# Optimization experiments

Hardware: AMD Instinct MI355X
Metric: run time of the kernel (lower is better)

The kernel has to match this reference:

```python
import jax, jax.numpy as jnp
import numpy as np

BATCH, T, N_STATE, N_IN, N_OUT = 256, 4096, 32, 8, 8
DT = 1e-3


def setup_inputs() -> dict:
    key = jax.random.key(0)
    k_u, k_x0, k_A, k_B, k_C, k_D = jax.random.split(key, 6)
    t = jnp.arange(T, dtype=jnp.float32) * DT
    u = jax.random.normal(k_u, (BATCH, T, N_IN), dtype=jnp.float32)
    x0 = jax.random.normal(k_x0, (BATCH, N_STATE), dtype=jnp.float32)
    # Stable-ish LTI system parameters
    A = (0.1 / np.sqrt(N_STATE)) * jax.random.normal(k_A, (N_STATE, N_STATE), dtype=jnp.float32) - 0.5 * jnp.eye(N_STATE, dtype=jnp.float32)
    B = jax.random.normal(k_B, (N_STATE, N_IN), dtype=jnp.float32) / np.sqrt(N_IN)
    C = jax.random.normal(k_C, (N_OUT, N_STATE), dtype=jnp.float32) / np.sqrt(N_STATE)
    D = jax.random.normal(k_D, (N_OUT, N_IN), dtype=jnp.float32) / np.sqrt(N_IN)
    return {"t": t, "u": u, "x0": x0, "A": A, "B": B, "C": C, "D": D}


def _dopri5_solve(t, u, x0, A, B):
    """Fixed-step Dopri5 (Dormand-Prince 5th order) on a uniform grid.

    Mirrors diffrax.diffeqsolve(Dopri5, ConstantStepSize, dt0=t[1], saveat=ts=t):
    one RK step per grid interval. u is evaluated at stage times via linear
    interpolation between grid samples.
    """
    dt = t[1] - t[0]

    def f(x, uu):  # vector field: dx = A x + B u
        return x @ A.T + uu @ B.T

    ut = jnp.swapaxes(u, 0, 1)  # [T, BATCH, N_IN]

    def step(x, uu):
        u0, u1 = uu
        du = u1 - u0
        k1 = f(x, u0)
        k2 = f(x + dt * (0.2 * k1), u0 + 0.2 * du)
        k3 = f(x + dt * (3.0 / 40.0 * k1 + 9.0 / 40.0 * k2), u0 + 0.3 * du)
        k4 = f(x + dt * (44.0 / 45.0 * k1 - 56.0 / 15.0 * k2 + 32.0 / 9.0 * k3), u0 + 0.8 * du)
        k5 = f(x + dt * (19372.0 / 6561.0 * k1 - 25360.0 / 2187.0 * k2 + 64448.0 / 6561.0 * k3 - 212.0 / 729.0 * k4), u0 + (8.0 / 9.0) * du)
        k6 = f(x + dt * (9017.0 / 3168.0 * k1 - 355.0 / 33.0 * k2 + 46732.0 / 5247.0 * k3 + 49.0 / 176.0 * k4 - 5103.0 / 18656.0 * k5), u1)
        xn = x + dt * (35.0 / 384.0 * k1 + 500.0 / 1113.0 * k3 + 125.0 / 192.0 * k4 - 2187.0 / 6784.0 * k5 + 11.0 / 84.0 * k6)
        return xn, xn

    _, xs_rest = jax.lax.scan(step, x0, (ut[:-1], ut[1:]))
    xs = jnp.concatenate([x0[None], xs_rest], axis=0)  # [T, BATCH, N_STATE]
    return jnp.swapaxes(xs, 0, 1)  # [BATCH, T, N_STATE]


def reference(t, u, x0, A, B, C, D):
    xs = _dopri5_solve(t, u, x0, A, B)          # state trajectory [BATCH, T, N_STATE]
    ys = xs @ C.T + u @ D.T                      # output y = C x + D u, [BATCH, T, N_OUT]
    return xs, ys
```

## Files before the change

### kernel.cpp

```cpp
#include <hip/hip_runtime.h>

#define BATCH 256
#define TT 4096
#define NS 32
#define NI 8
#define NO 8
#define LCH 64
#define NCHUNKS 64

#define WS_M  0
#define WS_N0 1024
#define WS_N1 1280
#define WS_ML 1536
#define WS_V  2560
#define WS_S  (2560 + BATCH * NCHUNKS * NS)

__device__ __forceinline__ float dot4(float4 a, float4 b) {
    return a.x * b.x + a.y * b.y + a.z * b.z + a.w * b.w;
}
__device__ __forceinline__ float4 ld4(const float* p) { return *(const float4*)p; }

__global__ __launch_bounds__(256) void k_pre(const float* __restrict__ tarr,
                                             const float* __restrict__ A,
                                             const float* __restrict__ B,
                                             float* __restrict__ ws) {
    __shared__ float sA[NS * NS], sB[NS * NI];
    __shared__ float Ka[6][NS * NS];
    __shared__ float Kb[6][NS * NI];
    __shared__ float Kc[6][NS * NI];
    __shared__ float Sa[NS * NS], Sb[NS * NI], Sc[NS * NI];
    __shared__ float Pq[2][NS * NS];

    const int tid = threadIdx.x;
    const float dt = tarr[1] - tarr[0];

    for (int e = tid; e < NS * NS; e += 256) sA[e] = A[e];
    for (int e = tid; e < NS * NI; e += 256) sB[e] = B[e];
    __syncthreads();
    for (int e = tid; e < NS * NS; e += 256) Ka[0][e] = sA[e];
    for (int e = tid; e < NS * NI; e += 256) { Kb[0][e] = sB[e]; Kc[0][e] = 0.f; }
    __syncthreads();

    const float atab[5][5] = {
        {0.2f, 0.f, 0.f, 0.f, 0.f},
        {3.f / 40.f, 9.f / 40.f, 0.f, 0.f, 0.f},
        {44.f / 45.f, -56.f / 15.f, 32.f / 9.f, 0.f, 0.f},
        {19372.f / 6561.f, -25360.f / 2187.f, 64448.f / 6561.f, -212.f / 729.f, 0.f},
        {9017.f / 3168.f, -355.f / 33.f, 46732.f / 5247.f, 49.f / 176.f, -5103.f / 18656.f}};
    const float ctab[6] = {0.f, 0.2f, 0.3f, 0.8f, 8.f / 9.f, 1.f};

    for (int st = 1; st <= 5; ++st) {
        for (int e = tid; e < NS * NS; e += 256) {
            float acc = 0.f;
            for (int j = 0; j < st; ++j) acc += atab[st - 1][j] * Ka[j][e];
            Sa[e] = acc;
        }
        for (int e = tid; e < NS * NI; e += 256) {
            float ab = 0.f, ac = 0.f;
            for (int j = 0; j < st; ++j) {
                ab += atab[st - 1][j] * Kb[j][e];
                ac += atab[st - 1][j] * Kc[j][e];
            }
            Sb[e] = ab; Sc[e] = ac;
        }
        __syncthreads();
        {
            const int j = tid & 31, ig = tid >> 5;
            for (int r = 0; r < 4; ++r) {
                const int row = ig + 8 * r;
                float acc = 0.f;
                for (int k = 0; k < NS; ++k) acc += sA[row * NS + k] * Sa[k * NS + j];
                Ka[st][row * NS + j] = sA[row * NS + j] + dt * acc;
            }
            const int jb = tid & 7, rb = tid >> 3;
            float ab = 0.f, ac = 0.f;
            for (int k = 0; k < NS; ++k) {
                ab += sA[rb * NS + k] * Sb[k * NI + jb];
                ac += sA[rb * NS + k] * Sc[k * NI + jb];
            }
            Kb[st][rb * NI + jb] = sB[rb * NI + jb] + dt * ab;
            Kc[st][rb * NI + jb] = ctab[st] * sB[rb * NI + jb] + dt * ac;
        }
        __syncthreads();
    }

    const float btab[6] = {35.f / 384.f, 0.f, 500.f / 1113.f, 125.f / 192.f,
                           -2187.f / 6784.f, 11.f / 84.f};
    for (int e = tid; e < NS * NS; e += 256) {
        float acc = 0.f;
        for (int i2 = 0; i2 < 6; ++i2) acc += btab[i2] * Ka[i2][e];
        const float m = dt * acc + (((e / NS) == (e % NS)) ? 1.f : 0.f);
        ws[WS_M + e] = m;
        Pq[0][e] = m;
    }
    for (int e = tid; e < NS * NI; e += 256) {
        float ap = 0.f, aq = 0.f;
        for (int i2 = 0; i2 < 6; ++i2) {
            ap += btab[i2] * Kb[i2][e];
            aq += btab[i2] * Kc[i2][e];
        }
        const float P = dt * ap, Q = dt * aq;
        ws[WS_N0 + e] = P - Q;
        ws[WS_N1 + e] = Q;
    }
    __syncthreads();

    int cur = 0;
    for (int itq = 0; itq < 6; ++itq) {
        const int j = tid & 31, ig = tid >> 5;
        for (int r = 0; r < 4; ++r) {
            const int row = ig + 8 * r;
            float acc = 0.f;
            for (int k = 0; k < NS; ++k) acc += Pq[cur][row * NS + k] * Pq[cur][k * NS + j];
            Pq[cur ^ 1][row * NS + j] = acc;
        }
        __syncthreads();
        cur ^= 1;
    }
    for (int e = tid; e < NS * NS; e += 256) ws[WS_ML + e] = Pq[cur][e];
}

template <bool P3>
__global__ __launch_bounds__(64, 1) void k_phase13(const float* __restrict__ u,
                                                   float* __restrict__ ws,
                                                   float* __restrict__ out,
                                                   const float* __restrict__ Cc,
                                                   const float* __restrict__ Dd) {
    const float* M = ws + WS_M;
    const float* N0 = ws + WS_N0;
    const float* N1 = ws + WS_N1;

    const int nch = P3 ? NCHUNKS : (NCHUNKS - 1);
    const int task = blockIdx.x;
    const int c = task % nch, g = task / nch;
    const int l = threadIdx.x;
    const int beta = l >> 3, s8 = l & 7;
    const int b = g * 8 + beta;

    float4 mq[4][8];
#pragma unroll
    for (int r = 0; r < 4; ++r)
#pragma unroll
        for (int jj = 0; jj < 8; ++jj) mq[r][jj] = ld4(M + (4 * s8 + r) * NS + 4 * jj);

    float4 n0q[4][2], n1q[4][2];
#pragma unroll
    for (int r = 0; r < 4; ++r) {
        n0q[r][0] = ld4(N0 + (4 * s8 + r) * NI);
        n0q[r][1] = ld4(N0 + (4 * s8 + r) * NI + 4);
        n1q[r][0] = ld4(N1 + (4 * s8 + r) * NI);
        n1q[r][1] = ld4(N1 + (4 * s8 + r) * NI + 4);
    }

    float4 cq[8], dq[2];
    if constexpr (P3) {
#pragma unroll
        for (int jj = 0; jj < 8; ++jj) cq[jj] = ld4(Cc + s8 * NS + 4 * jj);
        dq[0] = ld4(Dd + s8 * NI);
        dq[1] = ld4(Dd + s8 * NI + 4);
    }

    __shared__ float4 xb[2][8 * 9];

    const int t0 = c * LCH;
    const float* ub = u + (size_t)b * TT * NI;
    float4 u0a = ld4(ub + t0 * NI), u0b = ld4(ub + t0 * NI + 4);

    float4 mine;
    if constexpr (P3)
        mine = ld4(ws + WS_S + ((size_t)b * NCHUNKS + c) * NS + 4 * s8);
    else
        mine = make_float4(0.f, 0.f, 0.f, 0.f);

    xb[0][beta * 9 + s8] = mine;
    __syncthreads();

    float* yout = out + (size_t)BATCH * TT * NS;
    int cur = 0;
    for (int js = 0; js < LCH; ++js) {
        const int t = t0 + js;
        float4 xq[8];
#pragma unroll
        for (int jj = 0; jj < 8; ++jj) xq[jj] = xb[cur][beta * 9 + jj];

        if constexpr (P3) {
            *(float4*)(out + ((size_t)b * TT + t) * NS + 4 * s8) = mine;
            float yv = 0.f;
#pragma unroll
            for (int jj = 0; jj < 8; ++jj) yv += dot4(cq[jj], xq[jj]);
            yv += dot4(dq[0], u0a) + dot4(dq[1], u0b);
            yout[((size_t)b * TT + t) * NO + s8] = yv;
        }

        if (!P3 || js < LCH - 1) {
            const float4 u1a = ld4(ub + (t + 1) * NI);
            const float4 u1b = ld4(ub + (t + 1) * NI + 4);
            float w0 = dot4(n0q[0][0], u0a) + dot4(n0q[0][1], u0b) + dot4(n1q[0][0], u1a) + dot4(n1q[0][1], u1b);
            float w1 = dot4(n0q[1][0], u0a) + dot4(n0q[1][1], u0b) + dot4(n1q[1][0], u1a) + dot4(n1q[1][1], u1b);
            float w2 = dot4(n0q[2][0], u0a) + dot4(n0q[2][1], u0b) + dot4(n1q[2][0], u1a) + dot4(n1q[2][1], u1b);
            float w3 = dot4(n0q[3][0], u0a) + dot4(n0q[3][1], u0b) + dot4(n1q[3][0], u1a) + dot4(n1q[3][1], u1b);
#pragma unroll
            for (int jj = 0; jj < 8; ++jj) {
                const float4 xv = xq[jj];
                w0 += dot4(mq[0][jj], xv);
                w1 += dot4(mq[1][jj], xv);
                w2 += dot4(mq[2][jj], xv);
                w3 += dot4(mq[3][jj], xv);
            }
            mine = make_float4(w0, w1, w2, w3);
            xb[cur ^ 1][beta * 9 + s8] = mine;
            u0a = u1a;
            u0b = u1b;
        }
        __syncthreads();
        cur ^= 1;
    }

    if constexpr (!P3)
        *(float4*)(ws + WS_V + ((size_t)b * NCHUNKS + c) * NS + 4 * s8) = mine;
}

__global__ __launch_bounds__(64) void k_phase2(const float* __restrict__ x0,
                                               float* __restrict__ ws) {
    const float* ML = ws + WS_ML;
    const float* v = ws + WS_V;
    float* sst = ws + WS_S;
    const int b = blockIdx.x;
    const int l = threadIdx.x, i = l & 31, h = l >> 5;

    float mlr[16];
#pragma unroll
    for (int jj = 0; jj < 16; ++jj) mlr[jj] = ML[i * NS + 16 * h + jj];

    float x = x0[b * NS + i];
    for (int c = 0; c < NCHUNKS; ++c) {
        if (h == 0) sst[((size_t)b * NCHUNKS + c) * NS + i] = x;
        if (c == NCHUNKS - 1) break;
        float p = 0.f;
#pragma unroll
        for (int jj = 0; jj < 16; ++jj) p += mlr[jj] * __shfl(x, 16 * h + jj, 64);
        p += __shfl_xor(p, 32, 64);
        x = p + v[((size_t)b * NCHUNKS + c) * NS + i];
    }
}

extern "C" void kernel_launch(void* const* d_in, const int* in_sizes, int n_in,
                              void* d_out, int out_size, void* d_ws, size_t ws_size,
                              hipStream_t stream) {
    const float* t = (const float*)d_in[0];
    const float* u = (const float*)d_in[1];
    const float* x0 = (const float*)d_in[2];
    const float* A = (const float*)d_in[3];
    const float* B = (const float*)d_in[4];
    const float* C = (const float*)d_in[5];
    const float* D = (const float*)d_in[6];
    float* out = (float*)d_out;
    float* ws = (float*)d_ws;

    k_pre<<<dim3(1), dim3(256), 0, stream>>>(t, A, B, ws);
    k_phase13<false><<<dim3(32 * (NCHUNKS - 1)), dim3(64), 0, stream>>>(u, ws, out, C, D);
    k_phase2<<<dim3(BATCH), dim3(64), 0, stream>>>(x0, ws);
    k_phase13<true><<<dim3(32 * NCHUNKS), dim3(64), 0, stream>>>(u, ws, out, C, D);
}
```

Before: 414.9 us.

## Replace phase-1 sequential chunk scan with precomputed impulse-response convolution

Phase 1 no longer runs the 64-step recurrence per chunk from a zero state. k_pre now precomputes the per-lag input response matrices F_j (powers of M applied to N0/N1), and phase 1 becomes an independent weighted sum over the chunk's inputs, with no serial dependency. Phase 3 also replaces the block-wide __syncthreads with an lgkmcnt wait plus a sched barrier, which is enough because the block is a single 64-lane wavefront. It also prefetches u two steps ahead. The costs are a longer serial loop in the single-block k_pre and extra reads of F from the workspace.

```diff
diff --git a/kernel.cpp b/kernel.cpp
--- a/kernel.cpp
+++ b/kernel.cpp
@@ -14,6 +14,7 @@
 #define WS_ML 1536
 #define WS_V  2560
 #define WS_S  (2560 + BATCH * NCHUNKS * NS)
+#define WS_F  (WS_S + BATCH * NCHUNKS * NS)
 
 __device__ __forceinline__ float dot4(float4 a, float4 b) {
     return a.x * b.x + a.y * b.y + a.z * b.z + a.w * b.w;
@@ -30,6 +31,8 @@
     __shared__ float Kc[6][NS * NI];
     __shared__ float Sa[NS * NS], Sb[NS * NI], Sc[NS * NI];
     __shared__ float Pq[2][NS * NS];
+    __shared__ float Ms[NS * NS];
+    __shared__ float Ff[2][NS * NI];
 
     const int tid = threadIdx.x;
     const float dt = tarr[1] - tarr[0];
@@ -92,6 +95,7 @@
         const float m = dt * acc + (((e / NS) == (e % NS)) ? 1.f : 0.f);
         ws[WS_M + e] = m;
         Pq[0][e] = m;
+        Ms[e] = m;
     }
     for (int e = tid; e < NS * NI; e += 256) {
         float ap = 0.f, aq = 0.f;
@@ -102,6 +106,8 @@
         const float P = dt * ap, Q = dt * aq;
         ws[WS_N0 + e] = P - Q;
         ws[WS_N1 + e] = Q;
+        Sb[e] = P - Q;
+        Sc[e] = Q;
     }
     __syncthreads();
 
@@ -118,21 +124,86 @@
         cur ^= 1;
     }
     for (int e = tid; e < NS * NS; e += 256) ws[WS_ML + e] = Pq[cur][e];
-}
-
-template <bool P3>
-__global__ __launch_bounds__(64, 1) void k_phase13(const float* __restrict__ u,
-                                                   float* __restrict__ ws,
-                                                   float* __restrict__ out,
-                                                   const float* __restrict__ Cc,
-                                                   const float* __restrict__ Dd) {
+
+    Ff[0][tid] = Sc[tid];
+    ws[WS_F + 64 * NS * NI + tid] = Sc[tid];
+    __syncthreads();
+    int fc = 0;
+    const int rr = tid >> 3, mm = tid & 7;
+    for (int j = 63; j >= 0; --j) {
+        float acc = 0.f;
+#pragma unroll
+        for (int k = 0; k < NS; ++k) acc += Ms[rr * NS + k] * Ff[fc][k * NI + mm];
+        if (j == 63) acc += Sb[tid];
+        Ff[fc ^ 1][tid] = acc;
+        ws[WS_F + j * NS * NI + tid] = acc;
+        __syncthreads();
+        fc ^= 1;
+    }
+}
+
+__global__ __launch_bounds__(64) void k_phase1(const float* __restrict__ u,
+                                               float* __restrict__ ws) {
+    const float* F = ws + WS_F;
+    const int task = blockIdx.x;
+    const int c = task % (NCHUNKS - 1), g = task / (NCHUNKS - 1);
+    const int l = threadIdx.x;
+    const int beta = l >> 3, s8 = l & 7;
+    const int b = g * 8 + beta;
+    const int t0 = c * LCH;
+    const float* ub = u + ((size_t)b * TT + t0) * NI;
+    const float* Fp = F + 4 * s8 * NI;
+
+    float a0 = 0.f, a1 = 0.f, a2 = 0.f, a3 = 0.f;
+#pragma unroll 5
+    for (int j = 0; j <= LCH; ++j) {
+        const float4 ua = ld4(ub + j * NI);
+        const float4 uc = ld4(ub + j * NI + 4);
+        const float* Fj = Fp + j * (NS * NI);
+        a0 += dot4(ld4(Fj), ua) + dot4(ld4(Fj + 4), uc);
+        a1 += dot4(ld4(Fj + NI), ua) + dot4(ld4(Fj + NI + 4), uc);
+        a2 += dot4(ld4(Fj + 2 * NI), ua) + dot4(ld4(Fj + 2 * NI + 4), uc);
+        a3 += dot4(ld4(Fj + 3 * NI), ua) + dot4(ld4(Fj + 3 * NI + 4), uc);
+    }
+    *(float4*)(ws + WS_V + ((size_t)b * NCHUNKS + c) * NS + 4 * s8) =
+        make_float4(a0, a1, a2, a3);
+}
+
+__global__ __launch_bounds__(64) void k_phase2(const float* __restrict__ x0,
+                                               float* __restrict__ ws) {
+    const float* ML = ws + WS_ML;
+    const float* v = ws + WS_V;
+    float* sst = ws + WS_S;
+    const int b = blockIdx.x;
+    const int l = threadIdx.x, i = l & 31, h = l >> 5;
+
+    float mlr[16];
+#pragma unroll
+    for (int jj = 0; jj < 16; ++jj) mlr[jj] = ML[i * NS + 16 * h + jj];
+
+    float x = x0[b * NS + i];
+    for (int c = 0; c < NCHUNKS; ++c) {
+        if (h == 0) sst[((size_t)b * NCHUNKS + c) * NS + i] = x;
+        if (c == NCHUNKS - 1) break;
+        float p = 0.f;
+#pragma unroll
+        for (int jj = 0; jj < 16; ++jj) p += mlr[jj] * __shfl(x, 16 * h + jj, 64);
+        p += __shfl_xor(p, 32, 64);
+        x = p + v[((size_t)b * NCHUNKS + c) * NS + i];
+    }
+}
+
+__global__ __launch_bounds__(64, 1) void k_phase3(const float* __restrict__ u,
+                                                  float* __restrict__ ws,
+                                                  float* __restrict__ out,
+                                                  const float* __restrict__ Cc,
+                                                  const float* __restrict__ Dd) {
     const float* M = ws + WS_M;
     const float* N0 = ws + WS_N0;
     const float* N1 = ws + WS_N1;
 
-    const int nch = P3 ? NCHUNKS : (NCHUNKS - 1);
     const int task = blockIdx.x;
-    const int c = task % nch, g = task / nch;
+    const int c = task % NCHUNKS, g = task / NCHUNKS;
     const int l = threadIdx.x;
     const int beta = l >> 3, s8 = l & 7;
     const int b = g * 8 + beta;
@@ -153,27 +224,22 @@
     }
 
     float4 cq[8], dq[2];
-    if constexpr (P3) {
-#pragma unroll
-        for (int jj = 0; jj < 8; ++jj) cq[jj] = ld4(Cc + s8 * NS + 4 * jj);
-        dq[0] = ld4(Dd + s8 * NI);
-        dq[1] = ld4(Dd + s8 * NI + 4);
-    }
+#pragma unroll
+    for (int jj = 0; jj < 8; ++jj) cq[jj] = ld4(Cc + s8 * NS + 4 * jj);
+    dq[0] = ld4(Dd + s8 * NI);
+    dq[1] = ld4(Dd + s8 * NI + 4);
 
     __shared__ float4 xb[2][8 * 9];
 
     const int t0 = c * LCH;
     const float* ub = u + (size_t)b * TT * NI;
     float4 u0a = ld4(ub + t0 * NI), u0b = ld4(ub + t0 * NI + 4);
-
-    float4 mine;
-    if constexpr (P3)
-        mine = ld4(ws + WS_S + ((size_t)b * NCHUNKS + c) * NS + 4 * s8);
-    else
-        mine = make_float4(0.f, 0.f, 0.f, 0.f);
-
+    float4 u1a = ld4(ub + (t0 + 1) * NI), u1b = ld4(ub + (t0 + 1) * NI + 4);
+
+    float4 mine = ld4(ws + WS_S + ((size_t)b * NCHUNKS + c) * NS + 4 * s8);
     xb[0][beta * 9 + s8] = mine;
-    __syncthreads();
+    asm volatile("s_waitcnt lgkmcnt(0)" ::: "memory");
+    __builtin_amdgcn_sched_barrier(0);
 
     float* yout = out + (size_t)BATCH * TT * NS;
     int cur = 0;
@@ -183,18 +249,18 @@
 #pragma unroll
         for (int jj = 0; jj < 8; ++jj) xq[jj] = xb[cur][beta * 9 + jj];
 
-        if constexpr (P3) {
-            *(float4*)(out + ((size_t)b * TT + t) * NS + 4 * s8) = mine;
-            float yv = 0.f;
-#pragma unroll
-            for (int jj = 0; jj < 8; ++jj) yv += dot4(cq[jj], xq[jj]);
-            yv += dot4(dq[0], u0a) + dot4(dq[1], u0b);
-            yout[((size_t)b * TT + t) * NO + s8] = yv;
-        }
-
-        if (!P3 || js < LCH - 1) {
-            const float4 u1a = ld4(ub + (t + 1) * NI);
-            const float4 u1b = ld4(ub + (t + 1) * NI + 4);
+        const int tp = (t + 2 < TT - 1) ? (t + 2) : (TT - 1);
+        const float4 u2a = ld4(ub + tp * NI);
+        const float4 u2b = ld4(ub + tp * NI + 4);
+
+        *(float4*)(out + ((size_t)b * TT + t) * NS + 4 * s8) = mine;
+        float yv = 0.f;
+#pragma unroll
+        for (int jj = 0; jj < 8; ++jj) yv += dot4(cq[jj], xq[jj]);
+        yv += dot4(dq[0], u0a) + dot4(dq[1], u0b);
+        yout[((size_t)b * TT + t) * NO + s8] = yv;
+
+        if (js < LCH - 1) {
             float w0 = dot4(n0q[0][0], u0a) + dot4(n0q[0][1], u0b) + dot4(n1q[0][0], u1a) + dot4(n1q[0][1], u1b);
             float w1 = dot4(n0q[1][0], u0a) + dot4(n0q[1][1], u0b) + dot4(n1q[1][0], u1a) + dot4(n1q[1][1], u1b);
             float w2 = dot4(n0q[2][0], u0a) + dot4(n0q[2][1], u0b) + dot4(n1q[2][0], u1a) + dot4(n1q[2][1], u1b);
@@ -209,38 +275,12 @@
             }
             mine = make_float4(w0, w1, w2, w3);
             xb[cur ^ 1][beta * 9 + s8] = mine;
-            u0a = u1a;
-            u0b = u1b;
-        }
-        __syncthreads();
+            u0a = u1a; u0b = u1b;
+            u1a = u2a; u1b = u2b;
+        }
+        asm volatile("s_waitcnt lgkmcnt(0)" ::: "memory");
+        __builtin_amdgcn_sched_barrier(0);
         cur ^= 1;
-    }
-
-    if constexpr (!P3)
-        *(float4*)(ws + WS_V + ((size_t)b * NCHUNKS + c) * NS + 4 * s8) = mine;
-}
-
-__global__ __launch_bounds__(64) void k_phase2(const float* __restrict__ x0,
-                                               float* __restrict__ ws) {
-    const float* ML = ws + WS_ML;
-    const float* v = ws + WS_V;
-    float* sst = ws + WS_S;
-    const int b = blockIdx.x;
-    const int l = threadIdx.x, i = l & 31, h = l >> 5;
-
-    float mlr[16];
-#pragma unroll
-    for (int jj = 0; jj < 16; ++jj) mlr[jj] = ML[i * NS + 16 * h + jj];
-
-    float x = x0[b * NS + i];
-    for (int c = 0; c < NCHUNKS; ++c) {
-        if (h == 0) sst[((size_t)b * NCHUNKS + c) * NS + i] = x;
-        if (c == NCHUNKS - 1) break;
-        float p = 0.f;
-#pragma unroll
-        for (int jj = 0; jj < 16; ++jj) p += mlr[jj] * __shfl(x, 16 * h + jj, 64);
-        p += __shfl_xor(p, 32, 64);
-        x = p + v[((size_t)b * NCHUNKS + c) * NS + i];
     }
 }
 
@@ -258,7 +298,7 @@
     float* ws = (float*)d_ws;
 
     k_pre<<<dim3(1), dim3(256), 0, stream>>>(t, A, B, ws);
-    k_phase13<false><<<dim3(32 * (NCHUNKS - 1)), dim3(64), 0, stream>>>(u, ws, out, C, D);
+    k_phase1<<<dim3(32 * (NCHUNKS - 1)), dim3(64), 0, stream>>>(u, ws);
     k_phase2<<<dim3(BATCH), dim3(64), 0, stream>>>(x0, ws);
-    k_phase13<true><<<dim3(32 * NCHUNKS), dim3(64), 0, stream>>>(u, ws, out, C, D);
-}
+    k_phase3<<<dim3(32 * NCHUNKS), dim3(64), 0, stream>>>(u, ws, out, C, D);
+}
```

After: 449.2 us. 8.3% more time.
